# Performance work log

Hardware: AMD Instinct MI355X
Metric: run time of the kernel (lower is better)

## Reference

```python
import jax, jax.numpy as jnp
import numpy as np

N, C, R = 512, 32, 64   # atoms, feature channels, rbf count
EPS = 1e-8
GAMMA = 10.0
BOX = 10.0


def _eijk():
    e = np.zeros((3, 3, 3), dtype=np.float32)
    e[0, 1, 2] = e[1, 2, 0] = e[2, 0, 1] = 1.0
    e[0, 2, 1] = e[2, 1, 0] = e[1, 0, 2] = -1.0
    return jnp.asarray(e)


def setup_inputs() -> dict:
    key = jax.random.key(0)
    ks = jax.random.split(key, 8)
    d = {}
    d["geometry"] = jax.random.uniform(ks[0], (N, 3), dtype=jnp.float32) * BOX
    d["x0"] = jax.random.normal(ks[1], (N, C, 1), dtype=jnp.float32)
    d["x1"] = jax.random.normal(ks[2], (N, C, 3), dtype=jnp.float32)
    s1 = (6.0 / (R + R)) ** 0.5   # xavier_uniform for [R,R]
    s2 = (6.0 / (R + C)) ** 0.5   # xavier_uniform for [C,R]
    for i, name in enumerate(["f0", "fa", "fb", "fc"]):
        k1, k2 = jax.random.split(ks[3 + i])
        d[name + "_w1"] = jax.random.uniform(k1, (R, R), minval=-s1, maxval=s1, dtype=jnp.float32)
        d[name + "_b1"] = jnp.zeros((R,), jnp.float32)
        d[name + "_w2"] = jax.random.uniform(k2, (C, R), minval=-s2, maxval=s2, dtype=jnp.float32)
        d[name + "_b2"] = jnp.zeros((C,), jnp.float32)
    return d


def reference(geometry, x0, x1,
              f0_w1, f0_b1, f0_w2, f0_b2,
              fa_w1, fa_b1, fa_w2, fa_b2,
              fb_w1, fb_b1, fb_w2, fb_b2,
              fc_w1, fc_b1, fc_w2, fc_b2):
    # pairwise geometry: rij [N,N,3], squared dist r2 [N,N]
    rij = geometry[:, None, :] - geometry[None, :, :]
    r2 = jnp.sum(rij * rij, axis=-1)
    dij = jnp.sqrt(jnp.maximum(r2, EPS))                 # norm_with_epsilon
    centers = jnp.linspace(0.0, BOX, R, dtype=jnp.float32)
    rbf = jnp.exp(-GAMMA * (dij[..., None] - centers) ** 2)   # [N,N,R]

    self_mask = r2 < (EPS * EPS)                          # dij < EPS on true norm
    unit = rij / jnp.sqrt(r2 + EPS)[..., None]            # unit_vectors

    def radial(w1, b1, w2, b2):
        h = jax.nn.relu(jnp.einsum('abr,hr->abh', rbf, w1) + b1)
        return jnp.einsum('abh,ch->abc', h, w2) + b2      # [N,N,C]

    def f1(w1, b1, w2, b2):
        rad = jnp.where(self_mask[..., None], 0.0, radial(w1, b1, w2, b2))
        return unit[:, :, None, :] * rad[:, :, :, None]   # [N,N,C,3]

    # Filter_0 (shared radial weights) on l=0 and l=1 inputs: scalar filter, sum over neighbors b
    r0 = radial(f0_w1, f0_b1, f0_w2, f0_b2)               # [N,N,C]
    out0_a = jnp.einsum('abf,bfi->afi', r0, x0)           # [N,C,1] -> bucket 0
    out1_b = jnp.einsum('abf,bfi->afi', r0, x1)           # [N,C,3] -> bucket 1

    # filter_1_output_1 on l=0 input (cg = eye(3).unsqueeze(-1))
    F1a = f1(fa_w1, fa_b1, fa_w2, fa_b2)
    out1_a = jnp.einsum('abfi,bf->afi', F1a, x0[:, :, 0])  # [N,C,3]

    # filter_1_output_0 on l=1 input (cg = eye(3).unsqueeze(0))
    F1b = f1(fb_w1, fb_b1, fb_w2, fb_b2)
    out0_b = jnp.einsum('abfj,bfj->af', F1b, x1)[..., None]  # [N,C,1]

    # filter_1_output_1 on l=1 input (cg = eijk, cross-product coupling)
    F1c = f1(fc_w1, fc_b1, fc_w2, fc_b2)
    out1_c = jnp.einsum('ijk,abfj,bfk->afi', _eijk(), F1c, x1)  # [N,C,3]

    # concatenation() cats each bucket along channel axis (dim=-2)
    out0 = jnp.concatenate([out0_a, out0_b], axis=-2)      # [N,2C,1]
    out1 = jnp.concatenate([out1_a, out1_b, out1_c], axis=-2)  # [N,3C,3]
    return out0, out1
```

## Files before the change

kernel.cpp:

```cpp
#include <hip/hip_runtime.h>
#include <math.h>

namespace {

constexpr int NATOM = 512;
constexpr int BT    = 32;
constexpr int NT    = NATOM / BT;
constexpr float STEP = 10.0f / 63.0f;

typedef float f32x4 __attribute__((ext_vector_type(4)));
typedef short s16x8 __attribute__((ext_vector_type(8)));

struct Ptrs { const float* p[19]; };


__device__ __forceinline__ short f2bf(float f) {
  union { float f; unsigned u; } v; v.f = f;
  const unsigned r = (v.u + 0x7fffu + ((v.u >> 16) & 1u)) >> 16;
  return (short)r;
}

__global__ __launch_bounds__(256, 2)
void tfn_fused(Ptrs A, float* __restrict__ out) {
  const int a    = blockIdx.x;
  const int tid  = threadIdx.x;
  const int w    = tid >> 6;
  const int lane = tid & 63;
  const int ln   = lane & 15;
  const int hi   = lane >> 4;

  __shared__ __align__(16) short rbf_s[BT][72];
  __shared__ __align__(16) short h_s[4][BT][72];
  __shared__ __align__(16) float radT[128][36];
  __shared__ __align__(16) float x0T[32][36];
  __shared__ __align__(16) float x1T[96][36];
  __shared__ __align__(16) float uT[3][36];
  __shared__ __align__(16) float scr[96][5];

  const float* __restrict__ geom = A.p[0];
  const float* __restrict__ x0g  = A.p[1];
  const float* __restrict__ x1g  = A.p[2];

  s16x8 w1f[4][2];
  {
    const float* w1p = A.p[3 + 4 * w];
    #pragma unroll
    for (int nt = 0; nt < 4; ++nt)
      #pragma unroll
      for (int kt = 0; kt < 2; ++kt) {
        const float* src = w1p + (nt * 16 + ln) * 64 + kt * 32 + hi * 8;
        s16x8 f;
        #pragma unroll
        for (int i = 0; i < 8; ++i) f[i] = f2bf(src[i]);
        w1f[nt][kt] = f;
      }
  }
  float b1v[4];
  {
    const float* b1p = A.p[4 + 4 * w];
    #pragma unroll
    for (int nt = 0; nt < 4; ++nt) b1v[nt] = b1p[nt * 16 + ln];
  }
  s16x8 w2f[2][2];
  {
    const float* w2p = A.p[5 + 4 * w];
    #pragma unroll
    for (int nt = 0; nt < 2; ++nt)
      #pragma unroll
      for (int kt = 0; kt < 2; ++kt) {
        const float* src = w2p + (nt * 16 + ln) * 64 + kt * 32 + hi * 8;
        s16x8 f;
        #pragma unroll
        for (int i = 0; i < 8; ++i) f[i] = f2bf(src[i]);
        w2f[nt][kt] = f;
      }
  }
  float b2v[2];
  {
    const float* b2p = A.p[6 + 4 * w];
    #pragma unroll
    for (int nt = 0; nt < 2; ++nt) b2v[nt] = b2p[nt * 16 + ln];
  }

  const float gax = geom[3*a+0], gay = geom[3*a+1], gaz = geom[3*a+2];

  const bool act3 = (tid < 192);
  const int  t3   = (tid < 96) ? tid : tid - 96;
  const int  bh3  = (tid >= 96) ? 1 : 0;
  const int  c3   = t3 & 31;
  const int  i3   = t3 >> 5;
  const int  j3   = (i3 + 1) % 3;
  const int  k3   = (i3 + 2) % 3;

  float o1a = 0.f, o1b = 0.f, o1c = 0.f, o0a = 0.f, o0b = 0.f;

  for (int t = 0; t < NT; ++t) {
    const int b0 = t * BT;
    __syncthreads();

    {
      const int bb = tid & 31;
      const int rq = tid >> 5;
      const int bg = b0 + bb;
      const float dx = gax - geom[3*bg+0];
      const float dy = gay - geom[3*bg+1];
      const float dz = gaz - geom[3*bg+2];
      const float r2 = dx*dx + dy*dy + dz*dz;
      const float dij = sqrtf(fmaxf(r2, 1e-8f));
      const float base = dij - STEP * (float)(8 * rq);
      s16x8 pk;
      #pragma unroll
      for (int e = 0; e < 8; ++e) {
        const float d = base - STEP * (float)e;
        pk[e] = f2bf(__expf(-10.f * d * d));
      }
      *(s16x8*)&rbf_s[bb][rq * 8] = pk;
      if (rq == 0) {
        const float inv = 1.0f / sqrtf(r2 + 1e-8f);
        uT[0][bb] = dx * inv; uT[1][bb] = dy * inv; uT[2][bb] = dz * inv;
      }
      #pragma unroll
      for (int s = 0; s < 4; ++s) {
        const int idx = s * 256 + tid;
        x0T[idx & 31][idx >> 5] = x0g[b0 * 32 + idx];
      }
      #pragma unroll
      for (int s = 0; s < 12; ++s) {
        const int idx = s * 256 + tid;
        const int b = idx / 96, r = idx - b * 96;
        x1T[r][b] = x1g[b0 * 96 + idx];
      }
    }
    __syncthreads();

    {
      s16x8 af[2][2];
      #pragma unroll
      for (int mt = 0; mt < 2; ++mt)
        #pragma unroll
        for (int kt = 0; kt < 2; ++kt)
          af[mt][kt] = *(const s16x8*)&rbf_s[mt * 16 + ln][kt * 32 + hi * 8];
      f32x4 acc[2][4] = {};
      #pragma unroll
      for (int kt = 0; kt < 2; ++kt)
        #pragma unroll
        for (int mt = 0; mt < 2; ++mt)
          #pragma unroll
          for (int nt = 0; nt < 4; ++nt)
            acc[mt][nt] = __builtin_amdgcn_mfma_f32_16x16x32_bf16(
                af[mt][kt], w1f[nt][kt], acc[mt][nt], 0, 0, 0);
      #pragma unroll
      for (int mt = 0; mt < 2; ++mt)
        #pragma unroll
        for (int nt = 0; nt < 4; ++nt)
          #pragma unroll
          for (int r = 0; r < 4; ++r)
            h_s[w][mt * 16 + hi * 4 + r][nt * 16 + ln] =
                f2bf(fmaxf(acc[mt][nt][r] + b1v[nt], 0.0f));

      s16x8 a2[2][2];
      #pragma unroll
      for (int mt = 0; mt < 2; ++mt)
        #pragma unroll
        for (int kt = 0; kt < 2; ++kt)
          a2[mt][kt] = *(const s16x8*)&h_s[w][mt * 16 + ln][kt * 32 + hi * 8];
      f32x4 acc2[2][2] = {};
      #pragma unroll
      for (int kt = 0; kt < 2; ++kt)
        #pragma unroll
        for (int mt = 0; mt < 2; ++mt)
          #pragma unroll
          for (int nt = 0; nt < 2; ++nt)
            acc2[mt][nt] = __builtin_amdgcn_mfma_f32_16x16x32_bf16(
                a2[mt][kt], w2f[nt][kt], acc2[mt][nt], 0, 0, 0);
      #pragma unroll
      for (int mt = 0; mt < 2; ++mt)
        #pragma unroll
        for (int nt = 0; nt < 2; ++nt) {
          f32x4 v = acc2[mt][nt];
          #pragma unroll
          for (int r = 0; r < 4; ++r) v[r] += b2v[nt];
          *(f32x4*)&radT[w * 32 + nt * 16 + ln][mt * 16 + hi * 4] = v;
        }
    }
    __syncthreads();

    if (act3) {
      const int bB = bh3 * 16;
      #pragma unroll
      for (int bq = 0; bq < 4; ++bq) {
        const int bo = bB + bq * 4;
        const f32x4 r0 = *(const f32x4*)&radT[      c3][bo];
        const f32x4 ra = *(const f32x4*)&radT[32  + c3][bo];
        const f32x4 rb = *(const f32x4*)&radT[64  + c3][bo];
        const f32x4 rc = *(const f32x4*)&radT[96  + c3][bo];
        const f32x4 xv0 = *(const f32x4*)&x0T[c3][bo];
        const f32x4 xi  = *(const f32x4*)&x1T[3 * c3 + i3][bo];
        const f32x4 xj  = *(const f32x4*)&x1T[3 * c3 + j3][bo];
        const f32x4 xk  = *(const f32x4*)&x1T[3 * c3 + k3][bo];
        const f32x4 ui  = *(const f32x4*)&uT[i3][bo];
        const f32x4 uj  = *(const f32x4*)&uT[j3][bo];
        const f32x4 uk  = *(const f32x4*)&uT[k3][bo];
        #pragma unroll
        for (int e = 0; e < 4; ++e) {
          o1b = fmaf(r0[e], xi[e], o1b);
          o1a = fmaf(ra[e] * xv0[e], ui[e], o1a);
          o1c = fmaf(rc[e], fmaf(uj[e], xk[e], -(uk[e] * xj[e])), o1c);
          if (i3 == 0) {
            o0a = fmaf(r0[e], xv0[e], o0a);
            const float dot = fmaf(ui[e], xi[e], fmaf(uj[e], xj[e], uk[e] * xk[e]));
            o0b = fmaf(rb[e], dot, o0b);
          }
        }
      }
    }
  }

  __syncthreads();
  if (tid >= 96 && tid < 192) {
    const int q = tid - 96;
    scr[q][0] = o1a; scr[q][1] = o1b; scr[q][2] = o1c; scr[q][3] = o0a; scr[q][4] = o0b;
  }
  __syncthreads();
  if (tid < 96) {
    o1a += scr[tid][0]; o1b += scr[tid][1]; o1c += scr[tid][2];
    o0a += scr[tid][3]; o0b += scr[tid][4];
    float* o1 = out + NATOM * 64 + a * 288;
    o1[(      c3) * 3 + i3] = o1a;
    o1[(32  + c3) * 3 + i3] = o1b;
    o1[(64  + c3) * 3 + i3] = o1c;
    if (i3 == 0) {
      out[a * 64 + c3]      = o0a;
      out[a * 64 + 32 + c3] = o0b;
    }
  }
}

}

extern "C" void kernel_launch(void* const* d_in, const int* in_sizes, int n_in,
                              void* d_out, int out_size, void* d_ws, size_t ws_size,
                              hipStream_t stream) {
  (void)in_sizes; (void)n_in; (void)d_ws; (void)ws_size; (void)out_size;
  Ptrs A;
  for (int i = 0; i < 19; ++i) A.p[i] = (const float*)d_in[i];
  tfn_fused<<<dim3(NATOM), dim3(256), 0, stream>>>(A, (float*)d_out);
}
```

Measured before the change: 144.1 us.

## Split radial MLP across 8 waves and contract neighbors directly from MFMA registers

Moves to 512-thread blocks where each of 8 waves handles one filter and one 16-neighbor half. The contraction over neighbors now runs directly on the MFMA output registers, with x0/x1 read straight from global memory, so the radT/x0T/x1T LDS staging and one barrier per tile go away. It also double-buffers the rbf fragments, swizzles h_s to avoid bank conflicts, and finishes with a shuffle plus LDS reduction. The cost is more redundant global loads of x and more registers per thread, with launch bounds raised to 512 threads.

```diff
diff --git a/kernel.cpp b/kernel.cpp
--- a/kernel.cpp
+++ b/kernel.cpp
@@ -4,8 +4,6 @@
 namespace {
 
 constexpr int NATOM = 512;
-constexpr int BT    = 32;
-constexpr int NT    = NATOM / BT;
 constexpr float STEP = 10.0f / 63.0f;
 
 typedef float f32x4 __attribute__((ext_vector_type(4)));
@@ -14,28 +12,26 @@
 struct Ptrs { const float* p[19]; };
 
 
-__device__ __forceinline__ short f2bf(float f) {
+__device__ __forceinline__ unsigned f2bf(float f) {
   union { float f; unsigned u; } v; v.f = f;
-  const unsigned r = (v.u + 0x7fffu + ((v.u >> 16) & 1u)) >> 16;
-  return (short)r;
-}
-
-__global__ __launch_bounds__(256, 2)
+  return (v.u + 0x7fffu + ((v.u >> 16) & 1u)) >> 16;
+}
+
+__global__ __launch_bounds__(512, 4)
 void tfn_fused(Ptrs A, float* __restrict__ out) {
   const int a    = blockIdx.x;
   const int tid  = threadIdx.x;
-  const int w    = tid >> 6;
+  const int wv   = tid >> 6;
+  const int w    = wv & 3;
+  const int mh   = wv >> 2;
   const int lane = tid & 63;
   const int ln   = lane & 15;
   const int hi   = lane >> 4;
 
-  __shared__ __align__(16) short rbf_s[BT][72];
-  __shared__ __align__(16) short h_s[4][BT][72];
-  __shared__ __align__(16) float radT[128][36];
-  __shared__ __align__(16) float x0T[32][36];
-  __shared__ __align__(16) float x1T[96][36];
-  __shared__ __align__(16) float uT[3][36];
-  __shared__ __align__(16) float scr[96][5];
+  __shared__ __align__(16) short rbf_frag[2][2][2][64][8];
+  __shared__ __align__(16) float u_lds[2][32][4];
+  __shared__ __align__(16) short h_s[4 * 32 * 72];
+  __shared__ __align__(16) float scr[4][16][8];
 
   const float* __restrict__ geom = A.p[0];
   const float* __restrict__ x0g  = A.p[1];
@@ -51,7 +47,7 @@
         const float* src = w1p + (nt * 16 + ln) * 64 + kt * 32 + hi * 8;
         s16x8 f;
         #pragma unroll
-        for (int i = 0; i < 8; ++i) f[i] = f2bf(src[i]);
+        for (int i = 0; i < 8; ++i) f[i] = (short)f2bf(src[i]);
         w1f[nt][kt] = f;
       }
   }
@@ -71,167 +67,193 @@
         const float* src = w2p + (nt * 16 + ln) * 64 + kt * 32 + hi * 8;
         s16x8 f;
         #pragma unroll
-        for (int i = 0; i < 8; ++i) f[i] = f2bf(src[i]);
+        for (int i = 0; i < 8; ++i) f[i] = (short)f2bf(src[i]);
         w2f[nt][kt] = f;
       }
   }
   float b2v[2];
   {
     const float* b2p = A.p[6 + 4 * w];
-    #pragma unroll
-    for (int nt = 0; nt < 2; ++nt) b2v[nt] = b2p[nt * 16 + ln];
+    b2v[0] = b2p[ln]; b2v[1] = b2p[16 + ln];
   }
 
   const float gax = geom[3*a+0], gay = geom[3*a+1], gaz = geom[3*a+2];
 
-  const bool act3 = (tid < 192);
-  const int  t3   = (tid < 96) ? tid : tid - 96;
-  const int  bh3  = (tid >= 96) ? 1 : 0;
-  const int  c3   = t3 & 31;
-  const int  i3   = t3 >> 5;
-  const int  j3   = (i3 + 1) % 3;
-  const int  k3   = (i3 + 2) % 3;
-
-  float o1a = 0.f, o1b = 0.f, o1c = 0.f, o0a = 0.f, o0b = 0.f;
-
-  for (int t = 0; t < NT; ++t) {
-    const int b0 = t * BT;
-    __syncthreads();
+  float av[8] = {0.f,0.f,0.f,0.f,0.f,0.f,0.f,0.f};
+
+  for (int t = 0; t < 16; ++t) {
+    const int b0  = t * 32;
+    const int buf = t & 1;
+    const int bb4 = b0 + mh * 16 + hi * 4;
+
+    float x0r0[4], x1r0[4][3];
+    if (w <= 1) {
+      const float* p = x0g + bb4 * 32 + ln;
+      #pragma unroll
+      for (int e = 0; e < 4; ++e) x0r0[e] = p[e * 32];
+    }
+    if (w != 1) {
+      const float* p = x1g + bb4 * 96 + ln * 3;
+      #pragma unroll
+      for (int e = 0; e < 4; ++e) {
+        x1r0[e][0] = p[e*96+0]; x1r0[e][1] = p[e*96+1]; x1r0[e][2] = p[e*96+2];
+      }
+    }
 
     {
       const int bb = tid & 31;
-      const int rq = tid >> 5;
+      const int kq = tid >> 5;
       const int bg = b0 + bb;
       const float dx = gax - geom[3*bg+0];
       const float dy = gay - geom[3*bg+1];
       const float dz = gaz - geom[3*bg+2];
       const float r2 = dx*dx + dy*dy + dz*dz;
       const float dij = sqrtf(fmaxf(r2, 1e-8f));
-      const float base = dij - STEP * (float)(8 * rq);
-      s16x8 pk;
-      #pragma unroll
-      for (int e = 0; e < 8; ++e) {
-        const float d = base - STEP * (float)e;
-        pk[e] = f2bf(__expf(-10.f * d * d));
-      }
-      *(s16x8*)&rbf_s[bb][rq * 8] = pk;
-      if (rq == 0) {
+      const float d0 = dij - STEP * (float)(4 * kq);
+      const float d1 = d0 - STEP, d2 = d0 - 2.f*STEP, d3 = d0 - 3.f*STEP;
+      const unsigned lo = f2bf(__expf(-10.f*d0*d0)) | (f2bf(__expf(-10.f*d1*d1)) << 16);
+      const unsigned hi2 = f2bf(__expf(-10.f*d2*d2)) | (f2bf(__expf(-10.f*d3*d3)) << 16);
+      uint2 pk; pk.x = lo; pk.y = hi2;
+      *(uint2*)&rbf_frag[buf][kq >> 3][bb >> 4][((kq >> 1) & 3) * 16 + (bb & 15)][(kq & 1) * 4] = pk;
+      if (kq == 0) {
         const float inv = 1.0f / sqrtf(r2 + 1e-8f);
-        uT[0][bb] = dx * inv; uT[1][bb] = dy * inv; uT[2][bb] = dz * inv;
-      }
-      #pragma unroll
-      for (int s = 0; s < 4; ++s) {
-        const int idx = s * 256 + tid;
-        x0T[idx & 31][idx >> 5] = x0g[b0 * 32 + idx];
-      }
-      #pragma unroll
-      for (int s = 0; s < 12; ++s) {
-        const int idx = s * 256 + tid;
-        const int b = idx / 96, r = idx - b * 96;
-        x1T[r][b] = x1g[b0 * 96 + idx];
+        f32x4 uv; uv[0] = dx*inv; uv[1] = dy*inv; uv[2] = dz*inv; uv[3] = 0.f;
+        *(f32x4*)&u_lds[buf][bb][0] = uv;
       }
     }
     __syncthreads();
 
-    {
-      s16x8 af[2][2];
-      #pragma unroll
-      for (int mt = 0; mt < 2; ++mt)
+    const s16x8 af0 = *(const s16x8*)&rbf_frag[buf][0][mh][lane][0];
+    const s16x8 af1 = *(const s16x8*)&rbf_frag[buf][1][mh][lane][0];
+    f32x4 acc1[4] = {};
+    #pragma unroll
+    for (int nt = 0; nt < 4; ++nt)
+      acc1[nt] = __builtin_amdgcn_mfma_f32_16x16x32_bf16(af0, w1f[nt][0], acc1[nt], 0, 0, 0);
+    #pragma unroll
+    for (int nt = 0; nt < 4; ++nt)
+      acc1[nt] = __builtin_amdgcn_mfma_f32_16x16x32_bf16(af1, w1f[nt][1], acc1[nt], 0, 0, 0);
+    #pragma unroll
+    for (int nt = 0; nt < 4; ++nt) {
+      const int j = nt * 16 + ln;
+      #pragma unroll
+      for (int r = 0; r < 4; ++r) {
+        const int bl = mh * 16 + hi * 4 + r;
+        h_s[(w * 32 + bl) * 72 + (((j >> 3) ^ (bl & 7)) << 3) + (j & 7)] =
+            (short)f2bf(fmaxf(acc1[nt][r] + b1v[nt], 0.0f));
+      }
+    }
+
+    const int hbase = (w * 32 + mh * 16 + ln) * 72;
+    const s16x8 a20 = *(const s16x8*)&h_s[hbase + (((0 + hi) ^ (ln & 7)) << 3)];
+    const s16x8 a21 = *(const s16x8*)&h_s[hbase + (((4 + hi) ^ (ln & 7)) << 3)];
+    f32x4 acc2[2] = {};
+    acc2[0] = __builtin_amdgcn_mfma_f32_16x16x32_bf16(a20, w2f[0][0], acc2[0], 0, 0, 0);
+    acc2[1] = __builtin_amdgcn_mfma_f32_16x16x32_bf16(a20, w2f[1][0], acc2[1], 0, 0, 0);
+    acc2[0] = __builtin_amdgcn_mfma_f32_16x16x32_bf16(a21, w2f[0][1], acc2[0], 0, 0, 0);
+    acc2[1] = __builtin_amdgcn_mfma_f32_16x16x32_bf16(a21, w2f[1][1], acc2[1], 0, 0, 0);
+    float rad0[4], rad1[4];
+    #pragma unroll
+    for (int e = 0; e < 4; ++e) { rad0[e] = acc2[0][e] + b2v[0]; rad1[e] = acc2[1][e] + b2v[1]; }
+
+    float uu[4][3];
+    if (w != 0) {
+      #pragma unroll
+      for (int e = 0; e < 4; ++e) {
+        const f32x4 uv = *(const f32x4*)&u_lds[buf][mh * 16 + hi * 4 + e][0];
+        uu[e][0] = uv[0]; uu[e][1] = uv[1]; uu[e][2] = uv[2];
+      }
+    }
+    float x0r1[4], x1r1[4][3];
+    if (w <= 1) {
+      const float* p = x0g + bb4 * 32 + 16 + ln;
+      #pragma unroll
+      for (int e = 0; e < 4; ++e) x0r1[e] = p[e * 32];
+    }
+    if (w != 1) {
+      const float* p = x1g + bb4 * 96 + (16 + ln) * 3;
+      #pragma unroll
+      for (int e = 0; e < 4; ++e) {
+        x1r1[e][0] = p[e*96+0]; x1r1[e][1] = p[e*96+1]; x1r1[e][2] = p[e*96+2];
+      }
+    }
+
+    if (w == 0) {
+      #pragma unroll
+      for (int e = 0; e < 4; ++e) {
+        const float r = rad0[e];
+        av[0] = fmaf(r, x0r0[e],    av[0]);
+        av[1] = fmaf(r, x1r0[e][0], av[1]);
+        av[2] = fmaf(r, x1r0[e][1], av[2]);
+        av[3] = fmaf(r, x1r0[e][2], av[3]);
+        const float s = rad1[e];
+        av[4] = fmaf(s, x0r1[e],    av[4]);
+        av[5] = fmaf(s, x1r1[e][0], av[5]);
+        av[6] = fmaf(s, x1r1[e][1], av[6]);
+        av[7] = fmaf(s, x1r1[e][2], av[7]);
+      }
+    } else if (w == 1) {
+      #pragma unroll
+      for (int e = 0; e < 4; ++e) {
+        const float rx0 = rad0[e] * x0r0[e];
+        av[0] = fmaf(rx0, uu[e][0], av[0]);
+        av[1] = fmaf(rx0, uu[e][1], av[1]);
+        av[2] = fmaf(rx0, uu[e][2], av[2]);
+        const float rx1 = rad1[e] * x0r1[e];
+        av[3] = fmaf(rx1, uu[e][0], av[3]);
+        av[4] = fmaf(rx1, uu[e][1], av[4]);
+        av[5] = fmaf(rx1, uu[e][2], av[5]);
+      }
+    } else if (w == 2) {
+      #pragma unroll
+      for (int e = 0; e < 4; ++e) {
+        const float dot0 = fmaf(uu[e][0], x1r0[e][0], fmaf(uu[e][1], x1r0[e][1], uu[e][2] * x1r0[e][2]));
+        av[0] = fmaf(rad0[e], dot0, av[0]);
+        const float dot1 = fmaf(uu[e][0], x1r1[e][0], fmaf(uu[e][1], x1r1[e][1], uu[e][2] * x1r1[e][2]));
+        av[1] = fmaf(rad1[e], dot1, av[1]);
+      }
+    } else {
+      #pragma unroll
+      for (int e = 0; e < 4; ++e) {
         #pragma unroll
-        for (int kt = 0; kt < 2; ++kt)
-          af[mt][kt] = *(const s16x8*)&rbf_s[mt * 16 + ln][kt * 32 + hi * 8];
-      f32x4 acc[2][4] = {};
-      #pragma unroll
-      for (int kt = 0; kt < 2; ++kt)
-        #pragma unroll
-        for (int mt = 0; mt < 2; ++mt)
-          #pragma unroll
-          for (int nt = 0; nt < 4; ++nt)
-            acc[mt][nt] = __builtin_amdgcn_mfma_f32_16x16x32_bf16(
-                af[mt][kt], w1f[nt][kt], acc[mt][nt], 0, 0, 0);
-      #pragma unroll
-      for (int mt = 0; mt < 2; ++mt)
-        #pragma unroll
-        for (int nt = 0; nt < 4; ++nt)
-          #pragma unroll
-          for (int r = 0; r < 4; ++r)
-            h_s[w][mt * 16 + hi * 4 + r][nt * 16 + ln] =
-                f2bf(fmaxf(acc[mt][nt][r] + b1v[nt], 0.0f));
-
-      s16x8 a2[2][2];
-      #pragma unroll
-      for (int mt = 0; mt < 2; ++mt)
-        #pragma unroll
-        for (int kt = 0; kt < 2; ++kt)
-          a2[mt][kt] = *(const s16x8*)&h_s[w][mt * 16 + ln][kt * 32 + hi * 8];
-      f32x4 acc2[2][2] = {};
-      #pragma unroll
-      for (int kt = 0; kt < 2; ++kt)
-        #pragma unroll
-        for (int mt = 0; mt < 2; ++mt)
-          #pragma unroll
-          for (int nt = 0; nt < 2; ++nt)
-            acc2[mt][nt] = __builtin_amdgcn_mfma_f32_16x16x32_bf16(
-                a2[mt][kt], w2f[nt][kt], acc2[mt][nt], 0, 0, 0);
-      #pragma unroll
-      for (int mt = 0; mt < 2; ++mt)
-        #pragma unroll
-        for (int nt = 0; nt < 2; ++nt) {
-          f32x4 v = acc2[mt][nt];
-          #pragma unroll
-          for (int r = 0; r < 4; ++r) v[r] += b2v[nt];
-          *(f32x4*)&radT[w * 32 + nt * 16 + ln][mt * 16 + hi * 4] = v;
+        for (int i = 0; i < 3; ++i) {
+          const int j = (i + 1) % 3, k = (i + 2) % 3;
+          const float cr0 = fmaf(uu[e][j], x1r0[e][k], -(uu[e][k] * x1r0[e][j]));
+          av[i] = fmaf(rad0[e], cr0, av[i]);
+          const float cr1 = fmaf(uu[e][j], x1r1[e][k], -(uu[e][k] * x1r1[e][j]));
+          av[3 + i] = fmaf(rad1[e], cr1, av[3 + i]);
         }
-    }
-    __syncthreads();
-
-    if (act3) {
-      const int bB = bh3 * 16;
-      #pragma unroll
-      for (int bq = 0; bq < 4; ++bq) {
-        const int bo = bB + bq * 4;
-        const f32x4 r0 = *(const f32x4*)&radT[      c3][bo];
-        const f32x4 ra = *(const f32x4*)&radT[32  + c3][bo];
-        const f32x4 rb = *(const f32x4*)&radT[64  + c3][bo];
-        const f32x4 rc = *(const f32x4*)&radT[96  + c3][bo];
-        const f32x4 xv0 = *(const f32x4*)&x0T[c3][bo];
-        const f32x4 xi  = *(const f32x4*)&x1T[3 * c3 + i3][bo];
-        const f32x4 xj  = *(const f32x4*)&x1T[3 * c3 + j3][bo];
-        const f32x4 xk  = *(const f32x4*)&x1T[3 * c3 + k3][bo];
-        const f32x4 ui  = *(const f32x4*)&uT[i3][bo];
-        const f32x4 uj  = *(const f32x4*)&uT[j3][bo];
-        const f32x4 uk  = *(const f32x4*)&uT[k3][bo];
-        #pragma unroll
-        for (int e = 0; e < 4; ++e) {
-          o1b = fmaf(r0[e], xi[e], o1b);
-          o1a = fmaf(ra[e] * xv0[e], ui[e], o1a);
-          o1c = fmaf(rc[e], fmaf(uj[e], xk[e], -(uk[e] * xj[e])), o1c);
-          if (i3 == 0) {
-            o0a = fmaf(r0[e], xv0[e], o0a);
-            const float dot = fmaf(ui[e], xi[e], fmaf(uj[e], xj[e], uk[e] * xk[e]));
-            o0b = fmaf(rb[e], dot, o0b);
-          }
-        }
-      }
-    }
-  }
-
+      }
+    }
+  }
+
+  #pragma unroll
+  for (int q = 0; q < 8; ++q) {
+    av[q] += __shfl_xor(av[q], 16);
+    av[q] += __shfl_xor(av[q], 32);
+  }
+  if (mh == 1 && hi == 0) {
+    #pragma unroll
+    for (int q = 0; q < 8; ++q) scr[w][ln][q] = av[q];
+  }
   __syncthreads();
-  if (tid >= 96 && tid < 192) {
-    const int q = tid - 96;
-    scr[q][0] = o1a; scr[q][1] = o1b; scr[q][2] = o1c; scr[q][3] = o0a; scr[q][4] = o0b;
-  }
-  __syncthreads();
-  if (tid < 96) {
-    o1a += scr[tid][0]; o1b += scr[tid][1]; o1c += scr[tid][2];
-    o0a += scr[tid][3]; o0b += scr[tid][4];
+  if (mh == 0 && hi == 0) {
+    #pragma unroll
+    for (int q = 0; q < 8; ++q) av[q] += scr[w][ln][q];
     float* o1 = out + NATOM * 64 + a * 288;
-    o1[(      c3) * 3 + i3] = o1a;
-    o1[(32  + c3) * 3 + i3] = o1b;
-    o1[(64  + c3) * 3 + i3] = o1c;
-    if (i3 == 0) {
-      out[a * 64 + c3]      = o0a;
-      out[a * 64 + 32 + c3] = o0b;
+    if (w == 0) {
+      out[a * 64 + ln]      = av[0];
+      o1[(32 + ln) * 3 + 0] = av[1]; o1[(32 + ln) * 3 + 1] = av[2]; o1[(32 + ln) * 3 + 2] = av[3];
+      out[a * 64 + 16 + ln] = av[4];
+      o1[(48 + ln) * 3 + 0] = av[5]; o1[(48 + ln) * 3 + 1] = av[6]; o1[(48 + ln) * 3 + 2] = av[7];
+    } else if (w == 1) {
+      o1[(     ln) * 3 + 0] = av[0]; o1[(     ln) * 3 + 1] = av[1]; o1[(     ln) * 3 + 2] = av[2];
+      o1[(16 + ln) * 3 + 0] = av[3]; o1[(16 + ln) * 3 + 1] = av[4]; o1[(16 + ln) * 3 + 2] = av[5];
+    } else if (w == 2) {
+      out[a * 64 + 32 + ln] = av[0];
+      out[a * 64 + 48 + ln] = av[1];
+    } else {
+      o1[(64 + ln) * 3 + 0] = av[0]; o1[(64 + ln) * 3 + 1] = av[1]; o1[(64 + ln) * 3 + 2] = av[2];
+      o1[(80 + ln) * 3 + 0] = av[3]; o1[(80 + ln) * 3 + 1] = av[4]; o1[(80 + ln) * 3 + 2] = av[5];
     }
   }
 }
@@ -244,5 +266,5 @@
   (void)in_sizes; (void)n_in; (void)d_ws; (void)ws_size; (void)out_size;
   Ptrs A;
   for (int i = 0; i < 19; ++i) A.p[i] = (const float*)d_in[i];
-  tfn_fused<<<dim3(NATOM), dim3(256), 0, stream>>>(A, (float*)d_out);
-}
+  tfn_fused<<<dim3(NATOM), dim3(512), 0, stream>>>(A, (float*)d_out);
+}
```

Measured after the change: 305.6 us. +112.1%, slower.
